# Optimization experiments

Measured on AMD Instinct MI355X. Metric: run time of the kernel, lower is better.

The kernel has to match this reference:

```python
import jax, jax.numpy as jnp
import numpy as np

B, T, D = 1, 2048, 2048
HQ, HKV = 32, 8
DKV = 512  # HKV * head_dim

def setup_inputs() -> dict:
    key = jax.random.key(0)
    ks = jax.random.split(key, 5)
    s = 0.02
    return {
        "x": jax.random.normal(ks[0], (B, T, D), jnp.float32),
        "q_proj": jax.random.normal(ks[1], (D, D), jnp.float32) * s,
        "k_proj": jax.random.normal(ks[2], (DKV, D), jnp.float32) * s,
        "v_proj": jax.random.normal(ks[3], (DKV, D), jnp.float32) * s,
        "o_proj": jax.random.normal(ks[4], (D, D), jnp.float32) * s,
    }

def reference(x, q_proj, k_proj, v_proj, o_proj):
    b, t, _ = x.shape
    h_q, h_kv = HQ, HKV
    q_out = x @ q_proj.T            # [b,t,D]
    k_out = x @ k_proj.T            # [b,t,DKV]
    v_out = x @ v_proj.T
    dh_q = q_out.shape[-1] // h_q   # 64
    dh_k = k_out.shape[-1] // h_kv  # 64
    q = q_out.reshape(b, t, h_q, dh_q).transpose(0, 2, 1, 3)   # [b,hq,t,dh]
    k = k_out.reshape(b, t, h_kv, dh_k).transpose(0, 2, 1, 3)  # [b,hkv,t,dh]
    v = v_out.reshape(b, t, h_kv, dh_k).transpose(0, 2, 1, 3)
    group = h_q // h_kv
    k = jnp.repeat(k, group, axis=1)  # [b,hq,t,dh]
    v = jnp.repeat(v, group, axis=1)
    attn_logits = jnp.einsum('bhqd,bhkd->bhqk', q, k) / jnp.sqrt(jnp.float32(dh_q))
    mask = jnp.tril(jnp.ones((t, t), dtype=bool))
    attn = jax.nn.softmax(jnp.where(mask, attn_logits, -1e10), axis=-1)
    ctx = jnp.einsum('bhqk,bhkd->bhqd', attn, v)
    ctx = ctx.transpose(0, 2, 1, 3).reshape(b, t, o_proj.shape[0])
    return ctx @ o_proj
```

## Files before the change

kernel.cpp:

```cpp
#include <hip/hip_runtime.h>
#include <stdint.h>

typedef __attribute__((ext_vector_type(8))) __bf16 bf16x8;
typedef __attribute__((ext_vector_type(4))) float f32x4;
typedef __attribute__((ext_vector_type(4))) unsigned short u16x4;

typedef __attribute__((address_space(1))) unsigned int as1_uint;
typedef __attribute__((address_space(3))) unsigned int as3_uint;

__device__ __forceinline__ unsigned short f2bf(float f) {
  unsigned int u = __float_as_uint(f);
  u += 0x7fffu + ((u >> 16) & 1u);
  return (unsigned short)(u >> 16);
}

__device__ __forceinline__ void gload_lds16(const void* g, void* l) {
  __builtin_amdgcn_global_load_lds((as1_uint*)(uintptr_t)g, (as3_uint*)(uintptr_t)l,
                                   16, 0, 0);
}

__global__ void cvt_all(const float* __restrict__ x, const float* __restrict__ qp,
                        const float* __restrict__ kp, const float* __restrict__ vp,
                        unsigned short* __restrict__ xb, unsigned short* __restrict__ qpb,
                        unsigned short* __restrict__ kpb, unsigned short* __restrict__ vpb) {
  const int b = blockIdx.x;
  const float* in;
  unsigned short* out;
  int base;
  if (b < 4096)      { in = x;  out = xb;  base = b; }
  else if (b < 8192) { in = qp; out = qpb; base = b - 4096; }
  else if (b < 9216) { in = kp; out = kpb; base = b - 8192; }
  else               { in = vp; out = vpb; base = b - 9216; }
  const int i = base * 256 + threadIdx.x;
  float4 v = ((const float4*)in)[i];
  u16x4 o;
  o[0] = f2bf(v.x); o[1] = f2bf(v.y); o[2] = f2bf(v.z); o[3] = f2bf(v.w);
  ((u16x4*)out)[i] = o;
}

__global__ __launch_bounds__(256)
void transpose_cvt(const float* __restrict__ in, unsigned short* __restrict__ out,
                   int R, int C) {
  __shared__ unsigned short t[64][72];
  const int ti = blockIdx.y * 64;
  const int tj = blockIdx.x * 64;
  const int r  = threadIdx.x >> 4;
  const int c4 = (threadIdx.x & 15) * 4;
#pragma unroll
  for (int i = 0; i < 4; ++i) {
    int row = r + i * 16;
    float4 v = *(const float4*)&in[(size_t)(ti + row) * C + tj + c4];
    t[row][c4]     = f2bf(v.x);
    t[row][c4 + 1] = f2bf(v.y);
    t[row][c4 + 2] = f2bf(v.z);
    t[row][c4 + 3] = f2bf(v.w);
  }
  __syncthreads();
#pragma unroll
  for (int i = 0; i < 4; ++i) {
    int orow = r + i * 16;
    u16x4 o;
    o[0] = t[c4][orow]; o[1] = t[c4 + 1][orow];
    o[2] = t[c4 + 2][orow]; o[3] = t[c4 + 3][orow];
    *(u16x4*)&out[(size_t)(tj + orow) * R + ti + c4] = o;
  }
}

template <int BN, bool OUT_BF16>
__device__ __forceinline__
void gemm_body(const unsigned short* __restrict__ A,
               const unsigned short* __restrict__ B,
               void* __restrict__ Cout, int M, int N, int K, float alpha,
               int bx, int by, unsigned short* lA, unsigned short* lB) {
  constexpr int NF  = BN / 32;
  constexpr int ASZ = 64 * 64;
  constexpr int BSZ = BN * 64;
  const int tid  = threadIdx.x;
  const int lane = tid & 63;
  const int w    = tid >> 6;
  const int wr   = (w >> 1) * 32;
  const int wc   = (w & 1) * (BN / 2);
  const long brow = (long)by * 64;
  const long bcol = (long)bx * BN;
  const int lr = lane & 15;
  const int lq = lane >> 4;

  const int row0 = tid >> 3;
  const int lc0  = (tid & 7) ^ (row0 & 7);

  f32x4 acc[2][NF] = {};

  const unsigned short* gA = A + (brow + row0) * (long)K + lc0 * 8;
  const unsigned short* gB = B + (bcol + row0) * (long)K + lc0 * 8;

#define G_STAGE(buf, k0)                                                          \
  {                                                                               \
    gload_lds16(gA + (k0),           lA + (buf) * ASZ + tid * 8);                 \
    gload_lds16(gA + 32l * K + (k0), lA + (buf) * ASZ + 2048 + tid * 8);          \
    _Pragma("unroll")                                                             \
    for (int g = 0; g < NF; ++g)                                                  \
      gload_lds16(gB + g * 32l * K + (k0), lB + (buf) * BSZ + g * 2048 + tid * 8);\
  }

  G_STAGE(0, 0);
  __syncthreads();

  for (int k0 = 0; k0 < K; k0 += 64) {
    const int cur = (k0 >> 6) & 1;
    if (k0 + 64 < K) G_STAGE(cur ^ 1, k0 + 64);
#pragma unroll
    for (int kk = 0; kk < 2; ++kk) {
      const int j = kk * 4 + lq;
      const int ra0 = wr + lr, ra1 = wr + 16 + lr;
      bf16x8 a0 = *(const bf16x8*)&lA[cur * ASZ + ra0 * 64 + ((j ^ (ra0 & 7)) << 3)];
      bf16x8 a1 = *(const bf16x8*)&lA[cur * ASZ + ra1 * 64 + ((j ^ (ra1 & 7)) << 3)];
      bf16x8 b[NF];
#pragma unroll
      for (int n = 0; n < NF; ++n) {
        const int rb = wc + n * 16 + lr;
        b[n] = *(const bf16x8*)&lB[cur * BSZ + rb * 64 + ((j ^ (rb & 7)) << 3)];
      }
#pragma unroll
      for (int n = 0; n < NF; ++n) {
        acc[0][n] = __builtin_amdgcn_mfma_f32_16x16x32_bf16(a0, b[n], acc[0][n], 0, 0, 0);
        acc[1][n] = __builtin_amdgcn_mfma_f32_16x16x32_bf16(a1, b[n], acc[1][n], 0, 0, 0);
      }
    }
    __syncthreads();
  }
#undef G_STAGE

  const int orow = (int)brow + wr + lq * 4;
  const int ocol = (int)bcol + wc + lr;
#pragma unroll
  for (int m = 0; m < 2; ++m)
#pragma unroll
    for (int n = 0; n < NF; ++n)
#pragma unroll
      for (int r = 0; r < 4; ++r) {
        size_t row = (size_t)(orow + m * 16 + r);
        size_t col = (size_t)(ocol + n * 16);
        float v = acc[m][n][r] * alpha;
        if (OUT_BF16)
          ((unsigned short*)Cout)[row * N + col] = f2bf(v);
        else
          ((float*)Cout)[row * N + col] = v;
      }
}

template <int BN, bool OUT_BF16>
__global__ __launch_bounds__(256)
void gemm_nt(const unsigned short* __restrict__ A,
             const unsigned short* __restrict__ B,
             void* __restrict__ Cout, int M, int N, int K, float alpha) {
  __shared__ unsigned short lA[2 * 64 * 64];
  __shared__ unsigned short lB[2 * BN * 64];
  gemm_body<BN, OUT_BF16>(A, B, Cout, M, N, K, alpha, blockIdx.x, blockIdx.y, lA, lB);
}

__global__ __launch_bounds__(256)
void gemm_qk(const unsigned short* __restrict__ xb,
             const unsigned short* __restrict__ qpb,
             const unsigned short* __restrict__ kpb,
             unsigned short* __restrict__ Qb, unsigned short* __restrict__ Kbf) {
  __shared__ unsigned short lA[2 * 64 * 64];
  __shared__ unsigned short lB[2 * 128 * 64];
  const bool isQ = blockIdx.x < 16;
  const unsigned short* B = isQ ? qpb : kpb;
  unsigned short* C       = isQ ? Qb : Kbf;
  const int   N     = isQ ? 2048 : 512;
  const float alpha = isQ ? 0.125f * 1.44269504088896f : 1.0f;
  const int   bx    = isQ ? (int)blockIdx.x : (int)blockIdx.x - 16;
  gemm_body<128, true>(xb, B, C, 2048, N, 2048, alpha, bx, blockIdx.y, lA, lB);
}

__global__ __launch_bounds__(256)
void attn64(const unsigned short* __restrict__ Q,
            const unsigned short* __restrict__ Kb,
            const unsigned short* __restrict__ Vt,
            unsigned short* __restrict__ ctx) {
  constexpr int T = 2048, DQ = 2048, DKV = 512, DH = 64;
  const int h    = blockIdx.y;
  const int hkv  = h >> 2;
  const int tid  = threadIdx.x;
  const int lane = tid & 63;
  const int w    = tid >> 6;
  const int lr   = lane & 15;
  const int lq   = lane >> 4;
  const int lk   = lq * 8;
  const int sw   = lr & 7;

  __shared__ unsigned short lK[2][64 * 64];
  __shared__ unsigned short lV[2][64 * 64];
  __shared__ unsigned short P[4][16][72];

  const int row0 = tid >> 3;
  const int lc0  = (tid & 7) ^ (row0 & 7);

  bf16x8 ones_frag;
#pragma unroll
  for (int i = 0; i < 8; ++i) ones_frag[i] = (lr == 0) ? (__bf16)1.0f : (__bf16)0.0f;

#define STAGE_KV(bufidx, kv0)                                                        \
  {                                                                                  \
    gload_lds16(Kb + (size_t)((kv0) + row0) * DKV + hkv * DH + lc0 * 8,              \
                &lK[bufidx][tid * 8]);                                               \
    gload_lds16(Kb + (size_t)((kv0) + row0 + 32) * DKV + hkv * DH + lc0 * 8,         \
                &lK[bufidx][2048 + tid * 8]);                                        \
    gload_lds16(Vt + (size_t)(hkv * DH + row0) * T + (kv0) + lc0 * 8,                \
                &lV[bufidx][tid * 8]);                                               \
    gload_lds16(Vt + (size_t)(hkv * DH + row0 + 32) * T + (kv0) + lc0 * 8,           \
                &lV[bufidx][2048 + tid * 8]);                                        \
  }

#pragma unroll 1
  for (int pass = 0; pass < 2; ++pass) {
    const int qi  = pass == 0 ? (int)blockIdx.x : 31 - (int)blockIdx.x;
    const int q0b = qi * 64;
    const int qw  = q0b + w * 16;

    bf16x8 qf0 = *(const bf16x8*)&Q[(size_t)(qw + lr) * DQ + h * DH + lk];
    bf16x8 qf1 = *(const bf16x8*)&Q[(size_t)(qw + lr) * DQ + h * DH + 32 + lk];

    f32x4 oacc[4] = {};
    f32x4 lacc = {};
    float mr[4];
#pragma unroll
    for (int r = 0; r < 4; ++r) mr[r] = -3.0e38f;

    const int nt = qi + 1;
    STAGE_KV(0, 0);
    __syncthreads();

    for (int t = 0; t < nt; ++t) {
      const int kv0 = t * 64;
      const int cur = t & 1;
      if (t + 1 < nt) STAGE_KV(cur ^ 1, kv0 + 64);

      f32x4 s[4];
      __builtin_amdgcn_s_setprio(1);
#pragma unroll
      for (int n = 0; n < 4; ++n) {
        const int krow = n * 16 + lr;
        bf16x8 kf0 = *(const bf16x8*)&lK[cur][krow * 64 + ((lq ^ sw) << 3)];
        bf16x8 kf1 = *(const bf16x8*)&lK[cur][krow * 64 + (((4 + lq) ^ sw) << 3)];
        f32x4 acc = {};
        acc = __builtin_amdgcn_mfma_f32_16x16x32_bf16(qf0, kf0, acc, 0, 0, 0);
        acc = __builtin_amdgcn_mfma_f32_16x16x32_bf16(qf1, kf1, acc, 0, 0, 0);
        s[n] = acc;
      }
      __builtin_amdgcn_s_setprio(0);

      if (t == qi) {
        const int qr0 = qw + (lq << 2);
#pragma unroll
        for (int n = 0; n < 4; ++n) {
          int kc = kv0 + n * 16 + lr;
#pragma unroll
          for (int r = 0; r < 4; ++r)
            if (kc > qr0 + r) s[n][r] = -3.0e38f;
        }
      }

      float lml[4];
#pragma unroll
      for (int r = 0; r < 4; ++r)
        lml[r] = fmaxf(fmaxf(s[0][r], s[1][r]), fmaxf(s[2][r], s[3][r]));
      const bool defer = __all((lml[0] <= mr[0] + 8.f) & (lml[1] <= mr[1] + 8.f) &
                               (lml[2] <= mr[2] + 8.f) & (lml[3] <= mr[3] + 8.f));
      if (!defer) {
#pragma unroll
        for (int r = 0; r < 4; ++r) {
          float ml = lml[r];
          ml = fmaxf(ml, __shfl_xor(ml, 1));
          ml = fmaxf(ml, __shfl_xor(ml, 2));
          ml = fmaxf(ml, __shfl_xor(ml, 4));
          ml = fmaxf(ml, __shfl_xor(ml, 8));
          float mnew = fmaxf(mr[r], ml);
          float sc   = __builtin_amdgcn_exp2f(mr[r] - mnew);
          mr[r] = mnew;
          lacc[r] *= sc;
          oacc[0][r] *= sc; oacc[1][r] *= sc;
          oacc[2][r] *= sc; oacc[3][r] *= sc;
        }
      }

#pragma unroll
      for (int n = 0; n < 4; ++n)
#pragma unroll
        for (int r = 0; r < 4; ++r)
          s[n][r] = __builtin_amdgcn_exp2f(s[n][r] - mr[r]);

#pragma unroll
      for (int n = 0; n < 4; ++n)
#pragma unroll
        for (int r = 0; r < 4; ++r)
          P[w][(lq << 2) + r][n * 16 + lr] =
              (unsigned short)(__float_as_uint(s[n][r]) >> 16);
      asm volatile("s_waitcnt lgkmcnt(0)" ::: "memory");
      __builtin_amdgcn_sched_barrier(0);

      __builtin_amdgcn_s_setprio(1);
#pragma unroll
      for (int ks = 0; ks < 2; ++ks) {
        bf16x8 pf = *(const bf16x8*)&P[w][lr][ks * 32 + lk];
        lacc = __builtin_amdgcn_mfma_f32_16x16x32_bf16(pf, ones_frag, lacc, 0, 0, 0);
#pragma unroll
        for (int n = 0; n < 4; ++n) {
          const int vrow = n * 16 + lr;
          bf16x8 vf = *(const bf16x8*)&lV[cur][vrow * 64 + (((ks * 4 + lq) ^ sw) << 3)];
          oacc[n] = __builtin_amdgcn_mfma_f32_16x16x32_bf16(pf, vf, oacc[n], 0, 0, 0);
        }
      }
      __builtin_amdgcn_s_setprio(0);

      __syncthreads();
    }

    float inv[4];
#pragma unroll
    for (int r = 0; r < 4; ++r) {
      float l = __shfl(lacc[r], lane & 48);
      inv[r] = 1.f / l;
    }
#pragma unroll
    for (int n = 0; n < 4; ++n)
#pragma unroll
      for (int r = 0; r < 4; ++r) {
        int qrow = qw + (lq << 2) + r;
        ctx[(size_t)qrow * DQ + h * DH + n * 16 + lr] = f2bf(oacc[n][r] * inv[r]);
      }
  }
#undef STAGE_KV
}

extern "C" void kernel_launch(void* const* d_in, const int* in_sizes, int n_in,
                              void* d_out, int out_size, void* d_ws, size_t ws_size,
                              hipStream_t stream) {
  const float* x  = (const float*)d_in[0];
  const float* qp = (const float*)d_in[1];
  const float* kp = (const float*)d_in[2];
  const float* vp = (const float*)d_in[3];
  const float* op = (const float*)d_in[4];

  char* ws = (char*)d_ws;
  const size_t MB = 1024 * 1024;
  unsigned short* xb   = (unsigned short*)(ws + 0 * MB);
  unsigned short* qpb  = (unsigned short*)(ws + 8 * MB);
  unsigned short* kpb  = (unsigned short*)(ws + 16 * MB);
  unsigned short* vpb  = (unsigned short*)(ws + 18 * MB);
  unsigned short* opT  = (unsigned short*)(ws + 20 * MB);
  unsigned short* Qb   = (unsigned short*)(ws + 28 * MB);
  unsigned short* Kbf  = (unsigned short*)(ws + 36 * MB);
  unsigned short* Vtb  = (unsigned short*)(ws + 38 * MB);
  unsigned short* ctxb = (unsigned short*)(ws + 40 * MB);

  cvt_all<<<10240, 256, 0, stream>>>(x, qp, kp, vp, xb, qpb, kpb, vpb);
  transpose_cvt<<<dim3(32, 32), 256, 0, stream>>>(op, opT, 2048, 2048);

  gemm_qk<<<dim3(20, 32), 256, 0, stream>>>(xb, qpb, kpb, Qb, Kbf);
  gemm_nt<64, true><<<dim3(32, 8), 256, 0, stream>>>(vpb, xb, Vtb, 512, 2048, 2048, 1.0f);

  attn64<<<dim3(16, 32), 256, 0, stream>>>(Qb, Kbf, Vtb, ctxb);

  gemm_nt<128, false><<<dim3(16, 32), 256, 0, stream>>>(ctxb, opT, d_out, 2048, 2048, 2048, 1.0f);
}
```

Baseline: 131.5 us.

## Fuse Q/K/V projections into one launch and triple-buffer attention K/V loads

Merges the separate V-transpose projection GEMM into the Q/K projection kernel, giving a single 768-block launch with a flattened block index. This removes one kernel launch and lets all three projections share the machine. The attention kernel moves from double to triple buffering of K/V tiles, prefetching two tiles ahead, and replaces __syncthreads with explicit vmcnt waits plus s_barrier so loads stay in flight across iterations. It also swaps the grid order so the head index becomes blockIdx.x, changing block scheduling and cache locality. Costs are more LDS per block and hand-counted waitcnt values that must match the number of outstanding loads.

```diff
diff --git a/kernel.cpp b/kernel.cpp
--- a/kernel.cpp
+++ b/kernel.cpp
@@ -70,7 +70,7 @@
 __device__ __forceinline__
 void gemm_body(const unsigned short* __restrict__ A,
                const unsigned short* __restrict__ B,
-               void* __restrict__ Cout, int M, int N, int K, float alpha,
+               void* __restrict__ Cout, int N, int K, float alpha,
                int bx, int by, unsigned short* lA, unsigned short* lB) {
   constexpr int NF  = BN / 32;
   constexpr int ASZ = 64 * 64;
@@ -152,26 +152,39 @@
 __global__ __launch_bounds__(256)
 void gemm_nt(const unsigned short* __restrict__ A,
              const unsigned short* __restrict__ B,
-             void* __restrict__ Cout, int M, int N, int K, float alpha) {
+             void* __restrict__ Cout, int N, int K, float alpha) {
   __shared__ unsigned short lA[2 * 64 * 64];
   __shared__ unsigned short lB[2 * BN * 64];
-  gemm_body<BN, OUT_BF16>(A, B, Cout, M, N, K, alpha, blockIdx.x, blockIdx.y, lA, lB);
+  gemm_body<BN, OUT_BF16>(A, B, Cout, N, K, alpha, blockIdx.x, blockIdx.y, lA, lB);
 }
 
 __global__ __launch_bounds__(256)
-void gemm_qk(const unsigned short* __restrict__ xb,
-             const unsigned short* __restrict__ qpb,
-             const unsigned short* __restrict__ kpb,
-             unsigned short* __restrict__ Qb, unsigned short* __restrict__ Kbf) {
+void gemm_proj(const unsigned short* __restrict__ xb,
+               const unsigned short* __restrict__ qpb,
+               const unsigned short* __restrict__ kpb,
+               const unsigned short* __restrict__ vpb,
+               unsigned short* __restrict__ Qb, unsigned short* __restrict__ Kbf,
+               unsigned short* __restrict__ Vtb) {
   __shared__ unsigned short lA[2 * 64 * 64];
   __shared__ unsigned short lB[2 * 128 * 64];
-  const bool isQ = blockIdx.x < 16;
-  const unsigned short* B = isQ ? qpb : kpb;
-  unsigned short* C       = isQ ? Qb : Kbf;
-  const int   N     = isQ ? 2048 : 512;
-  const float alpha = isQ ? 0.125f * 1.44269504088896f : 1.0f;
-  const int   bx    = isQ ? (int)blockIdx.x : (int)blockIdx.x - 16;
-  gemm_body<128, true>(xb, B, C, 2048, N, 2048, alpha, bx, blockIdx.y, lA, lB);
+  const int bid = blockIdx.x;
+  const unsigned short *A, *B;
+  unsigned short* C;
+  int N, bx, by;
+  float alpha;
+  if (bid < 512) {
+    A = xb;  B = qpb; C = Qb;  N = 2048; alpha = 0.125f * 1.44269504088896f;
+    bx = bid & 15; by = bid >> 4;
+  } else if (bid < 640) {
+    int b = bid - 512;
+    A = xb;  B = kpb; C = Kbf; N = 512;  alpha = 1.0f;
+    bx = b & 3; by = b >> 2;
+  } else {
+    int b = bid - 640;
+    A = vpb; B = xb;  C = Vtb; N = 2048; alpha = 1.0f;
+    bx = b & 15; by = b >> 4;
+  }
+  gemm_body<128, true>(A, B, C, N, 2048, alpha, bx, by, lA, lB);
 }
 
 __global__ __launch_bounds__(256)
@@ -180,7 +193,7 @@
             const unsigned short* __restrict__ Vt,
             unsigned short* __restrict__ ctx) {
   constexpr int T = 2048, DQ = 2048, DKV = 512, DH = 64;
-  const int h    = blockIdx.y;
+  const int h    = blockIdx.x;
   const int hkv  = h >> 2;
   const int tid  = threadIdx.x;
   const int lane = tid & 63;
@@ -190,8 +203,8 @@
   const int lk   = lq * 8;
   const int sw   = lr & 7;
 
-  __shared__ unsigned short lK[2][64 * 64];
-  __shared__ unsigned short lV[2][64 * 64];
+  __shared__ unsigned short lK[3][64 * 64];
+  __shared__ unsigned short lV[3][64 * 64];
   __shared__ unsigned short P[4][16][72];
 
   const int row0 = tid >> 3;
@@ -215,7 +228,7 @@
 
 #pragma unroll 1
   for (int pass = 0; pass < 2; ++pass) {
-    const int qi  = pass == 0 ? (int)blockIdx.x : 31 - (int)blockIdx.x;
+    const int qi  = pass == 0 ? (int)blockIdx.y : 31 - (int)blockIdx.y;
     const int q0b = qi * 64;
     const int qw  = q0b + w * 16;
 
@@ -230,12 +243,20 @@
 
     const int nt = qi + 1;
     STAGE_KV(0, 0);
-    __syncthreads();
+    if (nt > 1) {
+      STAGE_KV(1, 64);
+      asm volatile("s_waitcnt vmcnt(4)" ::: "memory");
+    } else {
+      asm volatile("s_waitcnt vmcnt(0)" ::: "memory");
+    }
+    __builtin_amdgcn_sched_barrier(0);
+    __builtin_amdgcn_s_barrier();
 
     for (int t = 0; t < nt; ++t) {
       const int kv0 = t * 64;
-      const int cur = t & 1;
-      if (t + 1 < nt) STAGE_KV(cur ^ 1, kv0 + 64);
+      const int cur = t % 3;
+      const bool more = (t + 2 < nt);
+      if (more) STAGE_KV((t + 2) % 3, kv0 + 128);
 
       f32x4 s[4];
       __builtin_amdgcn_s_setprio(1);
@@ -314,7 +335,10 @@
       }
       __builtin_amdgcn_s_setprio(0);
 
-      __syncthreads();
+      if (more) asm volatile("s_waitcnt vmcnt(4)" ::: "memory");
+      else      asm volatile("s_waitcnt vmcnt(0)" ::: "memory");
+      __builtin_amdgcn_sched_barrier(0);
+      __builtin_amdgcn_s_barrier();
     }
 
     float inv[4];
@@ -358,10 +382,9 @@
   cvt_all<<<10240, 256, 0, stream>>>(x, qp, kp, vp, xb, qpb, kpb, vpb);
   transpose_cvt<<<dim3(32, 32), 256, 0, stream>>>(op, opT, 2048, 2048);
 
-  gemm_qk<<<dim3(20, 32), 256, 0, stream>>>(xb, qpb, kpb, Qb, Kbf);
-  gemm_nt<64, true><<<dim3(32, 8), 256, 0, stream>>>(vpb, xb, Vtb, 512, 2048, 2048, 1.0f);
-
-  attn64<<<dim3(16, 32), 256, 0, stream>>>(Qb, Kbf, Vtb, ctxb);
-
-  gemm_nt<128, false><<<dim3(16, 32), 256, 0, stream>>>(ctxb, opT, d_out, 2048, 2048, 2048, 1.0f);
-}
+  gemm_proj<<<768, 256, 0, stream>>>(xb, qpb, kpb, vpb, Qb, Kbf, Vtb);
+
+  attn64<<<dim3(32, 16), 256, 0, stream>>>(Qb, Kbf, Vtb, ctxb);
+
+  gemm_nt<128, false><<<dim3(16, 32), 256, 0, stream>>>(ctxb, opT, d_out, 2048, 2048, 1.0f);
+}
```

Measured after the change: 116.9 us, median of 3. 1.13x faster.
